# Optimization experiments

Hardware: AMD Instinct MI355X
Metric: run time of the kernel (lower is better)

Reference implementation:

```python
import jax, jax.numpy as jnp
import numpy as np

B, M, D = 512, 128, 512
N_ITER = 400      # FISTA iterations for batched NNLS (converges well past scipy nnls tol here)
POW_ITERS = 30    # power-iteration steps for spectral norm (Lipschitz constant)


def setup_inputs() -> dict:
    key = jax.random.key(0)
    k1, k2 = jax.random.split(key)
    pred_cost = jax.random.normal(k1, (B, D), dtype=jnp.float32)
    tight_ctrs = jax.random.normal(k2, (B, M, D), dtype=jnp.float32)
    return {"pred_cost": pred_cost, "tight_ctrs": tight_ctrs}


def _spectral_norm(G):
    # G: (B, M, M) PSD Gram matrices; power iteration -> largest eigenvalue per sample
    v = jnp.ones(G.shape[:-1], G.dtype)  # (B, M)
    def body(v, _):
        v = jnp.einsum('bij,bj->bi', G, v)
        v = v / (jnp.linalg.norm(v, axis=-1, keepdims=True) + 1e-12)
        return v, None
    v, _ = jax.lax.scan(body, v, None, length=POW_ITERS)
    Gv = jnp.einsum('bij,bj->bi', G, v)
    return jnp.linalg.norm(Gv, axis=-1)  # (B,)


def _batched_nnls(G, b, step):
    # Solve per-sample: min_{lam>=0} 0.5 lam^T G lam - b^T lam  (== ||ctr^T lam - p||^2 up to const)
    # FISTA with nonnegativity projection. G: (B,M,M), b: (B,M), step: (B,)
    lam0 = jnp.zeros_like(b)
    def body(carry, _):
        lam, y, t = carry
        grad = jnp.einsum('bij,bj->bi', G, y) - b
        lam_new = jnp.maximum(y - step[:, None] * grad, 0.0)
        t_new = 0.5 * (1.0 + jnp.sqrt(1.0 + 4.0 * t * t))
        y_new = lam_new + ((t - 1.0) / t_new) * (lam_new - lam)
        return (lam_new, y_new, t_new), None
    (lam, _, _), _ = jax.lax.scan(body, (lam0, lam0, jnp.float32(1.0)), None, length=N_ITER)
    return lam


def reference(pred_cost, tight_ctrs):
    # optmodel.modelSense == MINIMIZE -> flip sign of predicted cost
    p = -pred_cost  # (B, D)
    # drop (mask to zero) near-zero constraint rows: ctr[np.abs(ctr).sum(axis=1) > 1e-7]
    row_mask = jnp.sum(jnp.abs(tight_ctrs), axis=-1) > 1e-7  # (B, M)
    ctr = tight_ctrs * row_mask[..., None].astype(tight_ctrs.dtype)
    # NNLS: min_{lam>=0} ||ctr.T @ lam - p||^2, batched via normal equations
    G = jnp.einsum('bmd,bnd->bmn', ctr, ctr)   # (B, M, M)
    b = jnp.einsum('bmd,bd->bm', ctr, p)       # (B, M)
    L = _spectral_norm(G)
    step = 1.0 / jnp.maximum(L, 1e-12)
    lam = _batched_nnls(G, b, step)            # (B, M), lam >= 0
    proj = jnp.einsum('bm,bmd->bd', lam, ctr)  # (B, D) projection onto the cone
    proj = proj / (jnp.linalg.norm(proj, axis=-1, keepdims=True) + 1e-12)
    # projection is computed on detached numpy in the original -> constant wrt autograd
    proj = jax.lax.stop_gradient(proj)
    # loss = -cosine_similarity(p, proj), torch eps = 1e-8
    eps = jnp.float32(1e-8)
    pn = jnp.maximum(jnp.linalg.norm(p, axis=-1), eps)
    qn = jnp.maximum(jnp.linalg.norm(proj, axis=-1), eps)
    cos = jnp.sum(p * proj, axis=-1) / (pn * qn)
    return jnp.mean(-cos)  # reduction='mean'
```

## Files before the change

### kernel.cpp

```cpp
#include <hip/hip_runtime.h>
#include <math.h>

#define BATCH 512
#define M 128
#define D 512
#define PITER 9
#define NRUN 58
#define KC 64
#define NCH (D / KC)
#define SSTR 72
#define SCL 0.0009765625f

typedef __attribute__((ext_vector_type(8))) _Float16 h8;
typedef __attribute__((ext_vector_type(4))) float f4;
typedef __attribute__((ext_vector_type(2))) float v2f;

__device__ __forceinline__ float rdlane(float v, int k) {
    return __builtin_bit_cast(float, __builtin_amdgcn_readlane(__builtin_bit_cast(int, v), k));
}

__launch_bounds__(1024, 4)
__global__ void build_kernel(const float* __restrict__ pred,
                             const float* __restrict__ ctr,
                             float* __restrict__ Gw,
                             float* __restrict__ bw,
                             float* __restrict__ pw,
                             float* __restrict__ out)
{
    __shared__ __align__(16) _Float16 hiS[2][M * SSTR];
    __shared__ __align__(16) float p_s[D];
    __shared__ float mask_s[M];
    __shared__ float wred[16];

    const int tid = threadIdx.x;
    const int blk = blockIdx.x;
    const int w = tid >> 6, l = tid & 63;
    const int row = tid >> 3;
    const int seg = tid & 7;
    const int kk = 8 * seg;
    const int a = w >> 2;
    const int bcol = w & 3;
    const int fm = l & 15;
    const int fq = l >> 4;

    if (blk == 0 && tid == 0) out[0] = 0.0f;

    const float* predRow = pred + (size_t)blk * D;
    const float* ctrBase = ctr + (size_t)blk * (size_t)(M * D);

    float pv = (tid < D) ? predRow[tid] : 0.0f;
    if (tid < D) p_s[tid] = pv;
    float v = pv * pv;
    #pragma unroll
    for (int off = 32; off > 0; off >>= 1) v += __shfl_xor(v, off, 64);
    if (l == 0) wred[w] = v;
    __syncthreads();
    if (tid == 0) {
        float s = 0.0f;
        #pragma unroll
        for (int i = 0; i < 16; ++i) s += wred[i];
        pw[blk] = s;
    }

    f4 acc[2][2];
    #pragma unroll
    for (int i = 0; i < 2; ++i)
        #pragma unroll
        for (int jx = 0; jx < 2; ++jx)
            acc[i][jx] = (f4)0.0f;

    float rs = 0.0f, bp = 0.0f;
    const float* src = ctrBase + (size_t)row * D + kk;
    float4 f0 = *(const float4*)(src);
    float4 f1 = *(const float4*)(src + 4);

    for (int kc = 0; kc < NCH; ++kc) {
        const int cc = kc & 1;
        h8 hv = {(_Float16)f0.x, (_Float16)f0.y, (_Float16)f0.z, (_Float16)f0.w,
                 (_Float16)f1.x, (_Float16)f1.y, (_Float16)f1.z, (_Float16)f1.w};
        *(h8*)(hiS[cc] + row * SSTR + kk) = hv;
        rs += (fabsf(f0.x) + fabsf(f0.y) + fabsf(f0.z) + fabsf(f0.w))
            + (fabsf(f1.x) + fabsf(f1.y) + fabsf(f1.z) + fabsf(f1.w));
        {
            float4 pp0 = *(const float4*)(p_s + kc * KC + kk);
            float4 pp1 = *(const float4*)(p_s + kc * KC + kk + 4);
            bp += f0.x * pp0.x + f0.y * pp0.y + f0.z * pp0.z + f0.w * pp0.w
                + f1.x * pp1.x + f1.y * pp1.y + f1.z * pp1.z + f1.w * pp1.w;
        }
        __syncthreads();
        if (kc + 1 < NCH) {
            f0 = *(const float4*)(src + (kc + 1) * KC);
            f1 = *(const float4*)(src + (kc + 1) * KC + 4);
        }

        #pragma unroll
        for (int ks = 0; ks < 2; ++ks) {
            h8 Ah[2], Bh[2];
            #pragma unroll
            for (int t = 0; t < 2; ++t) {
                Ah[t] = *(const h8*)(hiS[cc] + (16 * (2 * a + t) + fm) * SSTR + 32 * ks + 8 * fq);
                Bh[t] = *(const h8*)(hiS[cc] + (16 * (2 * bcol + t) + fm) * SSTR + 32 * ks + 8 * fq);
            }
            #pragma unroll
            for (int al = 0; al < 2; ++al)
                #pragma unroll
                for (int be = 0; be < 2; ++be)
                    acc[al][be] = __builtin_amdgcn_mfma_f32_16x16x32_f16(Ah[al], Bh[be], acc[al][be], 0, 0, 0);
        }
    }

    rs += __shfl_xor(rs, 1, 64);
    rs += __shfl_xor(rs, 2, 64);
    rs += __shfl_xor(rs, 4, 64);
    bp += __shfl_xor(bp, 1, 64);
    bp += __shfl_xor(bp, 2, 64);
    bp += __shfl_xor(bp, 4, 64);
    if (seg == 0) {
        bool ok = rs > 1e-7f;
        mask_s[row] = ok ? 1.0f : 0.0f;
        bw[(size_t)blk * M + row] = ok ? -bp : 0.0f;
    }
    __syncthreads();

    float* Gb = Gw + (size_t)blk * (M * M);
    float mc0 = mask_s[32 * bcol + fm];
    float mc1 = mask_s[32 * bcol + 16 + fm];
    #pragma unroll
    for (int al = 0; al < 2; ++al)
        #pragma unroll
        for (int r = 0; r < 4; ++r) {
            const int grow = 32 * a + 16 * al + 4 * fq + r;
            const float mr_ = mask_s[grow];
            Gb[(size_t)grow * M + 32 * bcol + fm]      = acc[al][0][r] * mr_ * mc0;
            Gb[(size_t)grow * M + 32 * bcol + 16 + fm] = acc[al][1][r] * mr_ * mc1;
        }
}

__launch_bounds__(128, 1)
__global__ void solve_kernel(const float* __restrict__ Gw,
                             const float* __restrict__ bw,
                             const float* __restrict__ pw,
                             float* __restrict__ out)
{
    __shared__ __align__(16) v2f part[2][2][64];
    __shared__ float redA[2], redB[2];

    const int tid = threadIdx.x;
    const int wv = tid >> 6;
    const int l = tid & 63;
    const int blk = blockIdx.x;

    const float* g0 = Gw + (size_t)blk * (M * M) + (size_t)l * M + 64 * wv;
    const float* g1 = g0 + (size_t)64 * M;
    v2f g2[64];
    #pragma unroll
    for (int u = 0; u < 16; ++u) {
        f4 x = *(const f4*)(g0 + 4 * u);
        f4 y = *(const f4*)(g1 + 4 * u);
        g2[4 * u + 0] = v2f{x.x, y.x}; g2[4 * u + 1] = v2f{x.y, y.y};
        g2[4 * u + 2] = v2f{x.z, y.z}; g2[4 * u + 3] = v2f{x.w, y.w};
    }
    const float b_e = bw[(size_t)blk * M + 64 * wv + l];

    int mslot = 0;
    auto matvec = [&](float y_e) -> v2f {
        v2f acc[4];
        #pragma unroll
        for (int i = 0; i < 4; ++i) acc[i] = v2f{0.0f, 0.0f};
        #pragma unroll
        for (int k = 0; k < 64; ++k) {
            float s = rdlane(y_e, k);
            acc[k & 3] += g2[k] * v2f{s, s};
        }
        v2f p = (acc[0] + acc[1]) + (acc[2] + acc[3]);
        const int sl = mslot & 1; mslot++;
        part[sl][wv][l] = p;
        __syncthreads();
        return p + part[sl][1 - wv][l];
    };

    auto blockSum2 = [&](float x, float y, float& ox, float& oy) {
        #pragma unroll
        for (int off = 32; off > 0; off >>= 1) {
            x += __shfl_xor(x, off, 64);
            y += __shfl_xor(y, off, 64);
        }
        if (l == 0) { redA[wv] = x; redB[wv] = y; }
        __syncthreads();
        ox = redA[0] + redA[1];
        oy = redB[0] + redB[1];
        __syncthreads();
    };

    float v_e = 1.0f;
    for (int it = 0; it < PITER; ++it) {
        v2f u = matvec(v_e);
        v_e = ((wv == 0) ? u.x : u.y) * SCL;
    }
    float step;
    {
        v2f u = matvec(v_e);
        float u_e = (wv == 0) ? u.x : u.y;
        float nv, nu;
        blockSum2(v_e * v_e, u_e * u_e, nv, nu);
        float L = sqrtf(nu / fmaxf(nv, 1e-30f));
        step = 1.0f / fmaxf(1.15f * L, 1e-12f);
    }

    v2f st2 = v2f{step, step};
    #pragma unroll
    for (int k = 0; k < 64; ++k) g2[k] *= st2;
    const float bs = step * b_e;

    float lam = 0.0f, y = 0.0f, tk = 1.0f;
    for (int it = 0; it < NRUN; ++it) {
        v2f u = matvec(y);
        float u_e = (wv == 0) ? u.x : u.y;
        float tkn = 0.5f * (1.0f + sqrtf(1.0f + 4.0f * tk * tk));
        float bet = (tk - 1.0f) / tkn;
        float ln = fmaxf(y - u_e + bs, 0.0f);
        y = ln + bet * (ln - lam);
        lam = ln; tk = tkn;
    }

    {
        v2f u = matvec(lam);
        float u_e = (wv == 0) ? u.x : u.y;
        float sg, sb;
        blockSum2(lam * u_e, lam * b_e, sg, sb);
        if (tid == 0) {
            float glg = sg / step;
            float np_ = sqrtf(fmaxf(glg, 0.0f));
            float pdot = sb / (np_ + 1e-12f);
            float qn = fmaxf(np_ / (np_ + 1e-12f), 1e-8f);
            float pn = fmaxf(sqrtf(pw[blk]), 1e-8f);
            float c = pdot / (pn * qn);
            atomicAdd(out, -c * (1.0f / (float)BATCH));
        }
    }
}

extern "C" void kernel_launch(void* const* d_in, const int* in_sizes, int n_in,
                              void* d_out, int out_size, void* d_ws, size_t ws_size,
                              hipStream_t stream) {
    const float* pred = (const float*)d_in[0];
    const float* ctr  = (const float*)d_in[1];
    float* out = (float*)d_out;

    float* Gw = (float*)d_ws;
    float* bw = Gw + (size_t)BATCH * M * M;
    float* pw = bw + (size_t)BATCH * M;

    build_kernel<<<BATCH, 1024, 0, stream>>>(pred, ctr, Gw, bw, pw, out);
    solve_kernel<<<BATCH, 128, 0, stream>>>(Gw, bw, pw, out);
}
```

Before: 255.0 us.

## Fuse Gram build and FISTA solve into one kernel with LDS-resident G

Merges the build and solve kernels so each block keeps its 128x128 Gram matrix in shared memory instead of writing it to global workspace and reading it back. The solver now uses all 1024 threads: each row is split across 8 lanes holding 16 G entries in registers, with shuffle reductions and a double-buffered y vector in LDS. This removes the G round trip through global memory and the second launch, but adds a block-wide barrier per iteration across 16 waves and uses more LDS, which can lower occupancy. Output zeroing moves to a hipMemsetAsync.

```diff
diff --git a/kernel.cpp b/kernel.cpp
--- a/kernel.cpp
+++ b/kernel.cpp
@@ -9,28 +9,23 @@
 #define KC 64
 #define NCH (D / KC)
 #define SSTR 72
+#define GS 132
 #define SCL 0.0009765625f
 
 typedef __attribute__((ext_vector_type(8))) _Float16 h8;
 typedef __attribute__((ext_vector_type(4))) float f4;
-typedef __attribute__((ext_vector_type(2))) float v2f;
-
-__device__ __forceinline__ float rdlane(float v, int k) {
-    return __builtin_bit_cast(float, __builtin_amdgcn_readlane(__builtin_bit_cast(int, v), k));
-}
 
 __launch_bounds__(1024, 4)
-__global__ void build_kernel(const float* __restrict__ pred,
+__global__ void fused_kernel(const float* __restrict__ pred,
                              const float* __restrict__ ctr,
-                             float* __restrict__ Gw,
-                             float* __restrict__ bw,
-                             float* __restrict__ pw,
                              float* __restrict__ out)
 {
     __shared__ __align__(16) _Float16 hiS[2][M * SSTR];
     __shared__ __align__(16) float p_s[D];
+    __shared__ __align__(16) float G_s[M * GS];
+    __shared__ __align__(16) float y_s[2][M];
     __shared__ float mask_s[M];
-    __shared__ float wred[16];
+    __shared__ float wredA[16], wredB[16];
 
     const int tid = threadIdx.x;
     const int blk = blockIdx.x;
@@ -43,8 +38,6 @@
     const int fm = l & 15;
     const int fq = l >> 4;
 
-    if (blk == 0 && tid == 0) out[0] = 0.0f;
-
     const float* predRow = pred + (size_t)blk * D;
     const float* ctrBase = ctr + (size_t)blk * (size_t)(M * D);
 
@@ -53,13 +46,12 @@
     float v = pv * pv;
     #pragma unroll
     for (int off = 32; off > 0; off >>= 1) v += __shfl_xor(v, off, 64);
-    if (l == 0) wred[w] = v;
-    __syncthreads();
+    if (l == 0) wredA[w] = v;
+    __syncthreads();
+    float pn2 = 0.0f;
     if (tid == 0) {
-        float s = 0.0f;
-        #pragma unroll
-        for (int i = 0; i < 16; ++i) s += wred[i];
-        pw[blk] = s;
+        #pragma unroll
+        for (int i = 0; i < 16; ++i) pn2 += wredA[i];
     }
 
     f4 acc[2][2];
@@ -115,126 +107,119 @@
     bp += __shfl_xor(bp, 1, 64);
     bp += __shfl_xor(bp, 2, 64);
     bp += __shfl_xor(bp, 4, 64);
+    const bool okr = rs > 1e-7f;
+    const float b_e = okr ? -bp : 0.0f;
     if (seg == 0) {
-        bool ok = rs > 1e-7f;
-        mask_s[row] = ok ? 1.0f : 0.0f;
-        bw[(size_t)blk * M + row] = ok ? -bp : 0.0f;
-    }
-    __syncthreads();
-
-    float* Gb = Gw + (size_t)blk * (M * M);
-    float mc0 = mask_s[32 * bcol + fm];
-    float mc1 = mask_s[32 * bcol + 16 + fm];
+        mask_s[row] = okr ? 1.0f : 0.0f;
+        y_s[0][row] = 1.0f;
+    }
+    __syncthreads();
+
+    {
+        const float mc0 = mask_s[32 * bcol + fm];
+        const float mc1 = mask_s[32 * bcol + 16 + fm];
+        #pragma unroll
+        for (int al = 0; al < 2; ++al)
+            #pragma unroll
+            for (int r = 0; r < 4; ++r) {
+                const int grow = 32 * a + 16 * al + 4 * fq + r;
+                const float mr_ = mask_s[grow];
+                G_s[grow * GS + 32 * bcol + fm]      = acc[al][0][r] * mr_ * mc0;
+                G_s[grow * GS + 32 * bcol + 16 + fm] = acc[al][1][r] * mr_ * mc1;
+            }
+    }
+    __syncthreads();
+
+    int yoff[4];
     #pragma unroll
-    for (int al = 0; al < 2; ++al)
-        #pragma unroll
-        for (int r = 0; r < 4; ++r) {
-            const int grow = 32 * a + 16 * al + 4 * fq + r;
-            const float mr_ = mask_s[grow];
-            Gb[(size_t)grow * M + 32 * bcol + fm]      = acc[al][0][r] * mr_ * mc0;
-            Gb[(size_t)grow * M + 32 * bcol + 16 + fm] = acc[al][1][r] * mr_ * mc1;
-        }
-}
-
-__launch_bounds__(128, 1)
-__global__ void solve_kernel(const float* __restrict__ Gw,
-                             const float* __restrict__ bw,
-                             const float* __restrict__ pw,
-                             float* __restrict__ out)
-{
-    __shared__ __align__(16) v2f part[2][2][64];
-    __shared__ float redA[2], redB[2];
-
-    const int tid = threadIdx.x;
-    const int wv = tid >> 6;
-    const int l = tid & 63;
-    const int blk = blockIdx.x;
-
-    const float* g0 = Gw + (size_t)blk * (M * M) + (size_t)l * M + 64 * wv;
-    const float* g1 = g0 + (size_t)64 * M;
-    v2f g2[64];
-    #pragma unroll
-    for (int u = 0; u < 16; ++u) {
-        f4 x = *(const f4*)(g0 + 4 * u);
-        f4 y = *(const f4*)(g1 + 4 * u);
-        g2[4 * u + 0] = v2f{x.x, y.x}; g2[4 * u + 1] = v2f{x.y, y.y};
-        g2[4 * u + 2] = v2f{x.z, y.z}; g2[4 * u + 3] = v2f{x.w, y.w};
-    }
-    const float b_e = bw[(size_t)blk * M + 64 * wv + l];
-
-    int mslot = 0;
-    auto matvec = [&](float y_e) -> v2f {
-        v2f acc[4];
-        #pragma unroll
-        for (int i = 0; i < 4; ++i) acc[i] = v2f{0.0f, 0.0f};
-        #pragma unroll
-        for (int k = 0; k < 64; ++k) {
-            float s = rdlane(y_e, k);
-            acc[k & 3] += g2[k] * v2f{s, s};
-        }
-        v2f p = (acc[0] + acc[1]) + (acc[2] + acc[3]);
-        const int sl = mslot & 1; mslot++;
-        part[sl][wv][l] = p;
-        __syncthreads();
-        return p + part[sl][1 - wv][l];
+    for (int u4 = 0; u4 < 4; ++u4) yoff[u4] = 16 * seg + 4 * ((seg + u4) & 3);
+    const float* gp = G_s + row * GS;
+    f4 g0v = *(const f4*)(gp + yoff[0]);
+    f4 g1v = *(const f4*)(gp + yoff[1]);
+    f4 g2v = *(const f4*)(gp + yoff[2]);
+    f4 g3v = *(const f4*)(gp + yoff[3]);
+
+    int cur = 0;
+    auto matvec = [&]() -> float {
+        const float* yp = y_s[cur];
+        f4 a0 = g0v * (*(const f4*)(yp + yoff[0]));
+        f4 a1 = g1v * (*(const f4*)(yp + yoff[1]));
+        a0 += g2v * (*(const f4*)(yp + yoff[2]));
+        a1 += g3v * (*(const f4*)(yp + yoff[3]));
+        const f4 at = a0 + a1;
+        float u = (at.x + at.y) + (at.z + at.w);
+        u += __shfl_xor(u, 1, 64);
+        u += __shfl_xor(u, 2, 64);
+        u += __shfl_xor(u, 4, 64);
+        return u;
     };
-
+    auto publish = [&](float val) {
+        if (seg == 0) y_s[cur ^ 1][row] = val;
+        __syncthreads();
+        cur ^= 1;
+    };
     auto blockSum2 = [&](float x, float y, float& ox, float& oy) {
         #pragma unroll
-        for (int off = 32; off > 0; off >>= 1) {
+        for (int off = 1; off < 64; off <<= 1) {
             x += __shfl_xor(x, off, 64);
             y += __shfl_xor(y, off, 64);
         }
-        if (l == 0) { redA[wv] = x; redB[wv] = y; }
-        __syncthreads();
-        ox = redA[0] + redA[1];
-        oy = redB[0] + redB[1];
+        if (l == 0) { wredA[w] = x; wredB[w] = y; }
+        __syncthreads();
+        float sx = 0.0f, sy = 0.0f;
+        #pragma unroll
+        for (int i = 0; i < 16; ++i) { sx += wredA[i]; sy += wredB[i]; }
+        ox = sx; oy = sy;
         __syncthreads();
     };
 
     float v_e = 1.0f;
     for (int it = 0; it < PITER; ++it) {
-        v2f u = matvec(v_e);
-        v_e = ((wv == 0) ? u.x : u.y) * SCL;
+        const float u = matvec();
+        v_e = u * SCL;
+        publish(v_e);
     }
     float step;
     {
-        v2f u = matvec(v_e);
-        float u_e = (wv == 0) ? u.x : u.y;
+        const float u = matvec();
+        if (seg == 0) y_s[cur ^ 1][row] = 0.0f;
+        cur ^= 1;
         float nv, nu;
-        blockSum2(v_e * v_e, u_e * u_e, nv, nu);
-        float L = sqrtf(nu / fmaxf(nv, 1e-30f));
+        blockSum2((seg == 0) ? v_e * v_e : 0.0f,
+                  (seg == 0) ? u * u : 0.0f, nv, nu);
+        const float L = sqrtf(nu / fmaxf(nv, 1e-30f));
         step = 1.0f / fmaxf(1.15f * L, 1e-12f);
     }
 
-    v2f st2 = v2f{step, step};
-    #pragma unroll
-    for (int k = 0; k < 64; ++k) g2[k] *= st2;
+    g0v *= step; g1v *= step; g2v *= step; g3v *= step;
     const float bs = step * b_e;
 
-    float lam = 0.0f, y = 0.0f, tk = 1.0f;
+    float lam = 0.0f, yv = 0.0f, tk = 1.0f;
     for (int it = 0; it < NRUN; ++it) {
-        v2f u = matvec(y);
-        float u_e = (wv == 0) ? u.x : u.y;
-        float tkn = 0.5f * (1.0f + sqrtf(1.0f + 4.0f * tk * tk));
-        float bet = (tk - 1.0f) / tkn;
-        float ln = fmaxf(y - u_e + bs, 0.0f);
-        y = ln + bet * (ln - lam);
+        const float u = matvec();
+        const float tkn = 0.5f * (1.0f + sqrtf(1.0f + 4.0f * tk * tk));
+        const float bet = (tk - 1.0f) / tkn;
+        const float ln = fmaxf(yv - u + bs, 0.0f);
+        yv = ln + bet * (ln - lam);
         lam = ln; tk = tkn;
-    }
-
+        publish(yv);
+    }
+
+    if (seg == 0) y_s[cur ^ 1][row] = lam;
+    __syncthreads();
+    cur ^= 1;
     {
-        v2f u = matvec(lam);
-        float u_e = (wv == 0) ? u.x : u.y;
+        const float u = matvec();
         float sg, sb;
-        blockSum2(lam * u_e, lam * b_e, sg, sb);
+        blockSum2((seg == 0) ? lam * u : 0.0f,
+                  (seg == 0) ? lam * b_e : 0.0f, sg, sb);
         if (tid == 0) {
-            float glg = sg / step;
-            float np_ = sqrtf(fmaxf(glg, 0.0f));
-            float pdot = sb / (np_ + 1e-12f);
-            float qn = fmaxf(np_ / (np_ + 1e-12f), 1e-8f);
-            float pn = fmaxf(sqrtf(pw[blk]), 1e-8f);
-            float c = pdot / (pn * qn);
+            const float glg = sg / step;
+            const float np_ = sqrtf(fmaxf(glg, 0.0f));
+            const float pdot = sb / (np_ + 1e-12f);
+            const float qn = fmaxf(np_ / (np_ + 1e-12f), 1e-8f);
+            const float pn = fmaxf(sqrtf(pn2), 1e-8f);
+            const float c = pdot / (pn * qn);
             atomicAdd(out, -c * (1.0f / (float)BATCH));
         }
     }
@@ -247,10 +232,7 @@
     const float* ctr  = (const float*)d_in[1];
     float* out = (float*)d_out;
 
-    float* Gw = (float*)d_ws;
-    float* bw = Gw + (size_t)BATCH * M * M;
-    float* pw = bw + (size_t)BATCH * M;
-
-    build_kernel<<<BATCH, 1024, 0, stream>>>(pred, ctr, Gw, bw, pw, out);
-    solve_kernel<<<BATCH, 128, 0, stream>>>(Gw, bw, pw, out);
+    (void)d_ws; (void)ws_size;
+    hipMemsetAsync(d_out, 0, out_size, stream);
+    fused_kernel<<<BATCH, 1024, 0, stream>>>(pred, ctr, out);
 }
```

New measurement: 280.3 us. +9.9%, slower.
